# Optimization experiments

Measured on AMD Instinct MI355X. Metric: run time of the kernel, lower is better.

Reference implementation:

```python
import jax, jax.numpy as jnp
import numpy as np

DIM = 128
NUM_HEADS = 4
HEAD_DIM = DIM // NUM_HEADS
SCALE = HEAD_DIM ** -0.5


def setup_inputs() -> dict:
    key = jax.random.key(0)
    k1, k2, k3, k4, k5, k6 = jax.random.split(key, 6)
    BW, T = 8192, 49  # batch_windows, tokens per 7x7 window
    nW = 64           # distinct window masks; BW % nW == 0
    return {
        "x": jax.random.normal(k1, (BW, T, DIM), dtype=jnp.float32),
        "attention_mask": jax.random.normal(k2, (nW, T, T), dtype=jnp.float32),
        "w_qkv": jax.random.normal(k3, (3 * DIM, DIM), dtype=jnp.float32) * 0.02,
        "b_qkv": jax.random.normal(k4, (3 * DIM,), dtype=jnp.float32) * 0.02,
        "w_proj": jax.random.normal(k5, (DIM, DIM), dtype=jnp.float32) * 0.02,
        "b_proj": jax.random.normal(k6, (DIM,), dtype=jnp.float32) * 0.02,
    }


def reference(x, attention_mask, w_qkv, b_qkv, w_proj, b_proj):
    BW, T, C = x.shape
    H, hd = NUM_HEADS, HEAD_DIM
    # qkv projection: [BW, T, 3C] -> [3, BW, H, T, hd]
    qkv = (x @ w_qkv.T + b_qkv).reshape(BW, T, 3, H, hd)
    qkv = jnp.transpose(qkv, (2, 0, 3, 1, 4))
    q, k, v = qkv[0], qkv[1], qkv[2]
    # scaled dot-product scores: [BW, H, T, T]
    attn = jnp.einsum("bhqd,bhkd->bhqk", q * SCALE, k)
    nW = attention_mask.shape[0]
    # broadcast-add per-window mask over (batch, heads)
    attn = attn.reshape(-1, nW, H, T, T) + attention_mask[None, :, None, :, :]
    attn = attn.reshape(BW, H, T, T)
    attn = jax.nn.softmax(attn, axis=-1)
    out = jnp.einsum("bhqk,bhkd->bhqd", attn, v)  # [BW, H, T, hd]
    out = jnp.swapaxes(out, 1, 2).reshape(BW, T, C)
    return out @ w_proj.T + b_proj
```

## Files before the change

### kernel.cpp

```cpp
#include <hip/hip_runtime.h>
#include <hip/hip_bf16.h>


#define T49  49
#define CDIM 128
#define NW   64
#define SCALEF 0.17677669529663689f

typedef short bf16x8 __attribute__((ext_vector_type(8)));
typedef float f32x4  __attribute__((ext_vector_type(4)));

union B8 { unsigned int u[4]; bf16x8 v; };

__device__ __forceinline__ unsigned int pk2(float a, float b) {
  __hip_bfloat162 h = __float22bfloat162_rn(make_float2(a, b));
  unsigned int u;
  __builtin_memcpy(&u, &h, 4);
  return u;
}

__device__ __forceinline__ unsigned short f2bf(float f) {
  unsigned int u = __builtin_bit_cast(unsigned int, f);
  u += 0x7fffu + ((u >> 16) & 1u);
  return (unsigned short)(u >> 16);
}

__global__ void prep_kernel(const float* __restrict__ wq, const float* __restrict__ wp,
                            const float* __restrict__ mask,
                            short* __restrict__ wq_bf, short* __restrict__ wp_bf,
                            float* __restrict__ maskp) {
  const int i = blockIdx.x * 256 + threadIdx.x;
  const int w = i >> 12, q = (i >> 6) & 63, k = i & 63;
  float val = -3.0e38f;
  if (q < T49 && k < T49) val = mask[(w * T49 + q) * T49 + k];
  float rm = val;
  rm = fmaxf(rm, __shfl_xor(rm, 1, 64));
  rm = fmaxf(rm, __shfl_xor(rm, 2, 64));
  rm = fmaxf(rm, __shfl_xor(rm, 4, 64));
  rm = fmaxf(rm, __shfl_xor(rm, 8, 64));
  rm = fmaxf(rm, __shfl_xor(rm, 16, 64));
  rm = fmaxf(rm, __shfl_xor(rm, 32, 64));
  float mv;
  if (q >= T49)      mv = 0.0f;
  else if (k >= T49) mv = -1e30f;
  else               mv = val - rm;
  maskp[i] = mv;
  if (i < 3 * CDIM * CDIM) wq_bf[i] = (short)f2bf(wq[i]);
  if (i < CDIM * CDIM)     wp_bf[i] = (short)f2bf(wp[i]);
}

__global__ __launch_bounds__(256)
__attribute__((amdgpu_waves_per_eu(4, 4)))
void winattn_kernel(const float* __restrict__ x, const float* __restrict__ maskp,
                    const float* __restrict__ b_qkv, const float* __restrict__ b_proj,
                    const short* __restrict__ wq, const short* __restrict__ wp,
                    float* __restrict__ out) {
  __shared__ __align__(16) char smem[32768];
  constexpr int Q_BASE = 0, KO_BASE = 16384;

  const int bw    = blockIdx.x;
  const int wv    = threadIdx.x >> 6;
  const int lane  = threadIdx.x & 63;
  const int g     = lane >> 4;
  const int j16   = lane & 15;
  const int wmask = bw & (NW - 1);

  bf16x8 xa[4][4];
#pragma unroll
  for (int tt = 0; tt < 4; ++tt) {
    const int t = tt * 16 + j16;
#pragma unroll
    for (int kt = 0; kt < 4; ++kt) {
      B8 u;
      if (t < T49) {
        const float* p = x + (size_t)bw * (T49 * CDIM) + t * CDIM + kt * 32 + g * 8;
        const float4 v0 = *(const float4*)p;
        const float4 v1 = *(const float4*)(p + 4);
        u.u[0] = pk2(v0.x, v0.y); u.u[1] = pk2(v0.z, v0.w);
        u.u[2] = pk2(v1.x, v1.y); u.u[3] = pk2(v1.z, v1.w);
      } else {
        u.u[0] = u.u[1] = u.u[2] = u.u[3] = 0u;
      }
      xa[tt][kt] = u.v;
    }
  }

  unsigned int pkV[2][4][2];

#pragma unroll
  for (int ni = 0; ni < 6; ++ni) {
    const int ct = (ni < 2) ? (wv * 2 + ni)
                 : (ni < 4) ? (8 + wv * 2 + (ni - 2))
                            : (16 + wv * 2 + (ni - 4));
    bf16x8 wf[4];
#pragma unroll
    for (int kt = 0; kt < 4; ++kt)
      wf[kt] = *(const bf16x8*)(wq + (ct * 16 + j16) * CDIM + kt * 32 + g * 8);

    if (ni < 4) {
      const int  c0  = ct * 16 + g * 4;
      const bool isQ = (ni < 2);
      float4 b4 = *(const float4*)(b_qkv + c0);
      const float sc = isQ ? SCALEF : 1.0f;
      const int d0 = c0 & 31;
      char* base = smem + (isQ ? Q_BASE : KO_BASE) + wv * 4096;
#pragma unroll
      for (int tt = 0; tt < 4; ++tt) {
        f32x4 acc = {0.f, 0.f, 0.f, 0.f};
#pragma unroll
        for (int kt = 0; kt < 4; ++kt)
          acc = __builtin_amdgcn_mfma_f32_16x16x32_bf16(wf[kt], xa[tt][kt], acc, 0, 0, 0);
        const int t = tt * 16 + j16;
        const uint2 w2 = make_uint2(pk2(fmaf(acc[0], sc, b4.x * sc), fmaf(acc[1], sc, b4.y * sc)),
                                    pk2(fmaf(acc[2], sc, b4.z * sc), fmaf(acc[3], sc, b4.w * sc)));
        *(uint2*)(base + t * 64 + ((d0 * 2) ^ ((t & 3) << 4))) = w2;
      }
    } else {
      const int   vi   = ni - 4;
      const float bias = b_qkv[ct * 16 + j16];
#pragma unroll
      for (int tt = 0; tt < 4; ++tt) {
        f32x4 acc = {0.f, 0.f, 0.f, 0.f};
#pragma unroll
        for (int kt = 0; kt < 4; ++kt)
          acc = __builtin_amdgcn_mfma_f32_16x16x32_bf16(xa[tt][kt], wf[kt], acc, 0, 0, 0);
        pkV[vi][tt][0] = pk2(acc[0] + bias, acc[1] + bias);
        pkV[vi][tt][1] = pk2(acc[2] + bias, acc[3] + bias);
      }
    }
  }

  const int gh   = g >> 1;
  const int srcA = (((2 * g    ) & 3) << 4) | j16;
  const int srcB = (((2 * g + 1) & 3) << 4) | j16;

  const char* Kb = smem + KO_BASE + wv * 4096;
  const char* Qb = smem + Q_BASE  + wv * 4096;
  bf16x8 kb[4], qb[4];
#pragma unroll
  for (int mt = 0; mt < 4; ++mt) {
    const int t = mt * 16 + j16;
    kb[mt] = *(const bf16x8*)(Kb + t * 64 + ((g * 16) ^ ((t & 3) << 4)));
    qb[mt] = *(const bf16x8*)(Qb + t * 64 + ((g * 16) ^ ((t & 3) << 4)));
  }

  bf16x8 va[2][2];
#pragma unroll
  for (int dt = 0; dt < 2; ++dt)
#pragma unroll
    for (int ks = 0; ks < 2; ++ks) {
      const unsigned int a0  = (unsigned)__shfl((int)pkV[dt][2 * ks    ][0], srcA, 64);
      const unsigned int a0h = (unsigned)__shfl((int)pkV[dt][2 * ks + 1][0], srcA, 64);
      const unsigned int a1  = (unsigned)__shfl((int)pkV[dt][2 * ks    ][1], srcA, 64);
      const unsigned int a1h = (unsigned)__shfl((int)pkV[dt][2 * ks + 1][1], srcA, 64);
      const unsigned int b0  = (unsigned)__shfl((int)pkV[dt][2 * ks    ][0], srcB, 64);
      const unsigned int b0h = (unsigned)__shfl((int)pkV[dt][2 * ks + 1][0], srcB, 64);
      const unsigned int b1  = (unsigned)__shfl((int)pkV[dt][2 * ks    ][1], srcB, 64);
      const unsigned int b1h = (unsigned)__shfl((int)pkV[dt][2 * ks + 1][1], srcB, 64);
      B8 u;
      u.u[0] = gh ? a0h : a0;
      u.u[1] = gh ? a1h : a1;
      u.u[2] = gh ? b0h : b0;
      u.u[3] = gh ? b1h : b1;
      va[dt][ks] = u.v;
    }

  __syncthreads();

  char*        Ob  = smem + KO_BASE;
  const float* mwb = maskp + wmask * 4096;

#pragma unroll
  for (int nt = 0; nt < 4; ++nt) {
    const float* mp = mwb + (nt * 16 + j16) * 64 + g * 4;
    float4 m4[4];
#pragma unroll
    for (int mt = 0; mt < 4; ++mt) m4[mt] = *(const float4*)(mp + mt * 16);

    const f32x4 zero = {0.f, 0.f, 0.f, 0.f};
    float v[4][4];
#pragma unroll
    for (int mt = 0; mt < 4; ++mt) {
      const f32x4 s = __builtin_amdgcn_mfma_f32_16x16x32_bf16(kb[mt], qb[nt], zero, 0, 0, 0);
      v[mt][0] = __expf(s[0] + m4[mt].x); v[mt][1] = __expf(s[1] + m4[mt].y);
      v[mt][2] = __expf(s[2] + m4[mt].z); v[mt][3] = __expf(s[3] + m4[mt].w);
    }
    float sr[8];
#pragma unroll
    for (int mt = 0; mt < 4; ++mt) {
      sr[2 * mt]     = v[mt][0] + v[mt][1];
      sr[2 * mt + 1] = v[mt][2] + v[mt][3];
    }
    float sum = ((sr[0] + sr[1]) + (sr[2] + sr[3])) + ((sr[4] + sr[5]) + (sr[6] + sr[7]));
    sum += __shfl_xor(sum, 16, 64);
    sum += __shfl_xor(sum, 32, 64);
    const float inv = 1.0f / sum;

    unsigned int pkn[4][2];
#pragma unroll
    for (int mt = 0; mt < 4; ++mt) {
      pkn[mt][0] = pk2(v[mt][0], v[mt][1]);
      pkn[mt][1] = pk2(v[mt][2], v[mt][3]);
    }

    f32x4 oacc[2] = {{0.f,0.f,0.f,0.f},{0.f,0.f,0.f,0.f}};
#pragma unroll
    for (int ks = 0; ks < 2; ++ks) {
      const unsigned int p00 = (unsigned)__shfl((int)pkn[2*ks  ][0], srcA, 64);
      const unsigned int p10 = (unsigned)__shfl((int)pkn[2*ks+1][0], srcA, 64);
      const unsigned int p01 = (unsigned)__shfl((int)pkn[2*ks  ][1], srcA, 64);
      const unsigned int p11 = (unsigned)__shfl((int)pkn[2*ks+1][1], srcA, 64);
      const unsigned int q00 = (unsigned)__shfl((int)pkn[2*ks  ][0], srcB, 64);
      const unsigned int q10 = (unsigned)__shfl((int)pkn[2*ks+1][0], srcB, 64);
      const unsigned int q01 = (unsigned)__shfl((int)pkn[2*ks  ][1], srcB, 64);
      const unsigned int q11 = (unsigned)__shfl((int)pkn[2*ks+1][1], srcB, 64);
      B8 bf;
      bf.u[0] = gh ? p10 : p00;
      bf.u[1] = gh ? p11 : p01;
      bf.u[2] = gh ? q10 : q00;
      bf.u[3] = gh ? q11 : q01;
#pragma unroll
      for (int dt = 0; dt < 2; ++dt)
        oacc[dt] = __builtin_amdgcn_mfma_f32_16x16x32_bf16(va[dt][ks], bf.v, oacc[dt], 0, 0, 0);
    }

    const int to = nt * 16 + j16;
    const int sw = (to & 7) << 5;
#pragma unroll
    for (int dt = 0; dt < 2; ++dt) {
      const int ch0 = wv * 32 + dt * 16 + g * 4;
      const uint2 w2 = make_uint2(pk2(oacc[dt][0] * inv, oacc[dt][1] * inv),
                                  pk2(oacc[dt][2] * inv, oacc[dt][3] * inv));
      *(uint2*)(Ob + to * 256 + ((ch0 * 2) ^ sw)) = w2;
    }
  }
  __syncthreads();

  {
    const char* Ob2 = smem + KO_BASE;
    bf16x8 oa[4][4];
#pragma unroll
    for (int mt = 0; mt < 4; ++mt) {
      const int t = mt * 16 + j16;
      const int sw = (t & 7) << 5;
#pragma unroll
      for (int kt = 0; kt < 4; ++kt)
        oa[mt][kt] = *(const bf16x8*)(Ob2 + t * 256 + ((kt * 64 + g * 16) ^ sw));
    }
    float* ob = out + (size_t)bw * (T49 * CDIM);
#pragma unroll
    for (int ntl = 0; ntl < 2; ++ntl) {
      const int c = (wv * 2 + ntl) * 16 + j16;
      bf16x8 bfr[4];
#pragma unroll
      for (int kt = 0; kt < 4; ++kt)
        bfr[kt] = *(const bf16x8*)(wp + c * CDIM + kt * 32 + g * 8);
      const float bias = b_proj[c];
#pragma unroll
      for (int mt = 0; mt < 4; ++mt) {
        f32x4 acc = {0.f, 0.f, 0.f, 0.f};
#pragma unroll
        for (int kt = 0; kt < 4; ++kt)
          acc = __builtin_amdgcn_mfma_f32_16x16x32_bf16(oa[mt][kt], bfr[kt], acc, 0, 0, 0);
#pragma unroll
        for (int r = 0; r < 4; ++r) {
          const int t = mt * 16 + g * 4 + r;
          if (t < T49) ob[t * CDIM + c] = acc[r] + bias;
        }
      }
    }
  }
}

extern "C" void kernel_launch(void* const* d_in, const int* in_sizes, int n_in,
                              void* d_out, int out_size, void* d_ws, size_t ws_size,
                              hipStream_t stream) {
  const float* x      = (const float*)d_in[0];
  const float* mask   = (const float*)d_in[1];
  const float* w_qkv  = (const float*)d_in[2];
  const float* b_qkv  = (const float*)d_in[3];
  const float* w_proj = (const float*)d_in[4];
  const float* b_proj = (const float*)d_in[5];
  float* out = (float*)d_out;

  float* maskp = (float*)d_ws;
  short* wq_bf = (short*)((char*)d_ws + 64*64*64*4);
  short* wp_bf = wq_bf + 3 * CDIM * CDIM;

  hipLaunchKernelGGL(prep_kernel, dim3(1024), dim3(256), 0, stream,
                     w_qkv, w_proj, mask, wq_bf, wp_bf, maskp);
  hipLaunchKernelGGL(winattn_kernel, dim3(8192), dim3(256), 0, stream,
                     x, maskp, b_qkv, b_proj, wq_bf, wp_bf, out);
}
```

Baseline: 294.3 us.

## Stage x in LDS, move Q/K via shuffles, fold bias and mask into MFMA

The x tile is now converted to bf16 once and staged in a swizzled 16 KB LDS buffer instead of being held in registers. Q and K fragments are exchanged with cross-lane shuffles rather than through shared memory. The attention scale is folded into the bf16 Q weights during prep, and the biases and mask are passed as MFMA accumulator inputs. Together with the smaller LDS footprint and a relaxed waves-per-EU hint, this aims to cut register and LDS pressure and raise occupancy, at the cost of more shuffles and a block-wide barrier before the QKV projection.

```diff
diff --git a/kernel.cpp b/kernel.cpp
--- a/kernel.cpp
+++ b/kernel.cpp
@@ -45,18 +45,21 @@
   else if (k >= T49) mv = -1e30f;
   else               mv = val - rm;
   maskp[i] = mv;
-  if (i < 3 * CDIM * CDIM) wq_bf[i] = (short)f2bf(wq[i]);
-  if (i < CDIM * CDIM)     wp_bf[i] = (short)f2bf(wp[i]);
+  if (i < 3 * CDIM * CDIM) {
+    float wv_ = wq[i];
+    if (i < CDIM * CDIM) wv_ *= SCALEF;
+    wq_bf[i] = (short)f2bf(wv_);
+  }
+  if (i < CDIM * CDIM) wp_bf[i] = (short)f2bf(wp[i]);
 }
 
 __global__ __launch_bounds__(256)
-__attribute__((amdgpu_waves_per_eu(4, 4)))
+__attribute__((amdgpu_waves_per_eu(5)))
 void winattn_kernel(const float* __restrict__ x, const float* __restrict__ maskp,
                     const float* __restrict__ b_qkv, const float* __restrict__ b_proj,
                     const short* __restrict__ wq, const short* __restrict__ wp,
                     float* __restrict__ out) {
-  __shared__ __align__(16) char smem[32768];
-  constexpr int Q_BASE = 0, KO_BASE = 16384;
+  __shared__ __align__(16) char smem[16384];
 
   const int bw    = blockIdx.x;
   const int wv    = threadIdx.x >> 6;
@@ -65,26 +68,38 @@
   const int j16   = lane & 15;
   const int wmask = bw & (NW - 1);
 
-  bf16x8 xa[4][4];
-#pragma unroll
-  for (int tt = 0; tt < 4; ++tt) {
+  {
+    const int tid = threadIdx.x;
+    const int t   = tid >> 2;
+    const int c0  = (tid & 3) * 32;
+    char* wb = smem + t * 256;
+    const int swz = (t & 7) << 4;
+    if (t < T49) {
+      const float* p = x + (size_t)bw * (T49 * CDIM) + t * CDIM + c0;
+#pragma unroll
+      for (int q = 0; q < 4; ++q) {
+        const float4 v0 = *(const float4*)(p + q * 8);
+        const float4 v1 = *(const float4*)(p + q * 8 + 4);
+        uint4 u;
+        u.x = pk2(v0.x, v0.y); u.y = pk2(v0.z, v0.w);
+        u.z = pk2(v1.x, v1.y); u.w = pk2(v1.z, v1.w);
+        *(uint4*)(wb + ((c0 * 2 + q * 16) ^ swz)) = u;
+      }
+    } else {
+#pragma unroll
+      for (int q = 0; q < 4; ++q)
+        *(uint4*)(wb + ((c0 * 2 + q * 16) ^ swz)) = make_uint4(0u, 0u, 0u, 0u);
+    }
+  }
+  __syncthreads();
+
+  auto XF = [&](int tt, int kt) -> bf16x8 {
     const int t = tt * 16 + j16;
-#pragma unroll
-    for (int kt = 0; kt < 4; ++kt) {
-      B8 u;
-      if (t < T49) {
-        const float* p = x + (size_t)bw * (T49 * CDIM) + t * CDIM + kt * 32 + g * 8;
-        const float4 v0 = *(const float4*)p;
-        const float4 v1 = *(const float4*)(p + 4);
-        u.u[0] = pk2(v0.x, v0.y); u.u[1] = pk2(v0.z, v0.w);
-        u.u[2] = pk2(v1.x, v1.y); u.u[3] = pk2(v1.z, v1.w);
-      } else {
-        u.u[0] = u.u[1] = u.u[2] = u.u[3] = 0u;
-      }
-      xa[tt][kt] = u.v;
-    }
-  }
-
+    return *(const bf16x8*)(smem + t * 256 + ((kt * 64 + g * 16) ^ ((t & 7) << 4)));
+  };
+
+  unsigned int pkQ[2][4][2];
+  unsigned int pkK[2][4][2];
   unsigned int pkV[2][4][2];
 
 #pragma unroll
@@ -98,34 +113,35 @@
       wf[kt] = *(const bf16x8*)(wq + (ct * 16 + j16) * CDIM + kt * 32 + g * 8);
 
     if (ni < 4) {
-      const int  c0  = ct * 16 + g * 4;
-      const bool isQ = (ni < 2);
+      const int   c0 = ct * 16 + g * 4;
       float4 b4 = *(const float4*)(b_qkv + c0);
-      const float sc = isQ ? SCALEF : 1.0f;
-      const int d0 = c0 & 31;
-      char* base = smem + (isQ ? Q_BASE : KO_BASE) + wv * 4096;
+      if (ni < 2) { b4.x *= SCALEF; b4.y *= SCALEF; b4.z *= SCALEF; b4.w *= SCALEF; }
+      const f32x4 cin = {b4.x, b4.y, b4.z, b4.w};
 #pragma unroll
       for (int tt = 0; tt < 4; ++tt) {
-        f32x4 acc = {0.f, 0.f, 0.f, 0.f};
+        f32x4 acc = cin;
 #pragma unroll
         for (int kt = 0; kt < 4; ++kt)
-          acc = __builtin_amdgcn_mfma_f32_16x16x32_bf16(wf[kt], xa[tt][kt], acc, 0, 0, 0);
-        const int t = tt * 16 + j16;
-        const uint2 w2 = make_uint2(pk2(fmaf(acc[0], sc, b4.x * sc), fmaf(acc[1], sc, b4.y * sc)),
-                                    pk2(fmaf(acc[2], sc, b4.z * sc), fmaf(acc[3], sc, b4.w * sc)));
-        *(uint2*)(base + t * 64 + ((d0 * 2) ^ ((t & 3) << 4))) = w2;
+          acc = __builtin_amdgcn_mfma_f32_16x16x32_bf16(wf[kt], XF(tt, kt), acc, 0, 0, 0);
+        unsigned int p0 = pk2(acc[0], acc[1]);
+        unsigned int p1 = pk2(acc[2], acc[3]);
+        if (ni == 0)      { pkQ[0][tt][0] = p0; pkQ[0][tt][1] = p1; }
+        else if (ni == 1) { pkQ[1][tt][0] = p0; pkQ[1][tt][1] = p1; }
+        else if (ni == 2) { pkK[0][tt][0] = p0; pkK[0][tt][1] = p1; }
+        else              { pkK[1][tt][0] = p0; pkK[1][tt][1] = p1; }
       }
     } else {
       const int   vi   = ni - 4;
       const float bias = b_qkv[ct * 16 + j16];
+      const f32x4 cin = {bias, bias, bias, bias};
 #pragma unroll
       for (int tt = 0; tt < 4; ++tt) {
-        f32x4 acc = {0.f, 0.f, 0.f, 0.f};
+        f32x4 acc = cin;
 #pragma unroll
         for (int kt = 0; kt < 4; ++kt)
-          acc = __builtin_amdgcn_mfma_f32_16x16x32_bf16(xa[tt][kt], wf[kt], acc, 0, 0, 0);
-        pkV[vi][tt][0] = pk2(acc[0] + bias, acc[1] + bias);
-        pkV[vi][tt][1] = pk2(acc[2] + bias, acc[3] + bias);
+          acc = __builtin_amdgcn_mfma_f32_16x16x32_bf16(XF(tt, kt), wf[kt], acc, 0, 0, 0);
+        pkV[vi][tt][0] = pk2(acc[0], acc[1]);
+        pkV[vi][tt][1] = pk2(acc[2], acc[3]);
       }
     }
   }
@@ -134,14 +150,41 @@
   const int srcA = (((2 * g    ) & 3) << 4) | j16;
   const int srcB = (((2 * g + 1) & 3) << 4) | j16;
 
-  const char* Kb = smem + KO_BASE + wv * 4096;
-  const char* Qb = smem + Q_BASE  + wv * 4096;
-  bf16x8 kb[4], qb[4];
+  bf16x8 qb[4], kb[4];
 #pragma unroll
   for (int mt = 0; mt < 4; ++mt) {
-    const int t = mt * 16 + j16;
-    kb[mt] = *(const bf16x8*)(Kb + t * 64 + ((g * 16) ^ ((t & 3) << 4)));
-    qb[mt] = *(const bf16x8*)(Qb + t * 64 + ((g * 16) ^ ((t & 3) << 4)));
+    {
+      const unsigned int a0 = (unsigned)__shfl((int)pkQ[0][mt][0], srcA, 64);
+      const unsigned int a1 = (unsigned)__shfl((int)pkQ[0][mt][1], srcA, 64);
+      const unsigned int c0 = (unsigned)__shfl((int)pkQ[1][mt][0], srcA, 64);
+      const unsigned int c1 = (unsigned)__shfl((int)pkQ[1][mt][1], srcA, 64);
+      const unsigned int b0 = (unsigned)__shfl((int)pkQ[0][mt][0], srcB, 64);
+      const unsigned int b1 = (unsigned)__shfl((int)pkQ[0][mt][1], srcB, 64);
+      const unsigned int d0 = (unsigned)__shfl((int)pkQ[1][mt][0], srcB, 64);
+      const unsigned int d1 = (unsigned)__shfl((int)pkQ[1][mt][1], srcB, 64);
+      B8 u;
+      u.u[0] = gh ? c0 : a0;
+      u.u[1] = gh ? c1 : a1;
+      u.u[2] = gh ? d0 : b0;
+      u.u[3] = gh ? d1 : b1;
+      qb[mt] = u.v;
+    }
+    {
+      const unsigned int a0 = (unsigned)__shfl((int)pkK[0][mt][0], srcA, 64);
+      const unsigned int a1 = (unsigned)__shfl((int)pkK[0][mt][1], srcA, 64);
+      const unsigned int c0 = (unsigned)__shfl((int)pkK[1][mt][0], srcA, 64);
+      const unsigned int c1 = (unsigned)__shfl((int)pkK[1][mt][1], srcA, 64);
+      const unsigned int b0 = (unsigned)__shfl((int)pkK[0][mt][0], srcB, 64);
+      const unsigned int b1 = (unsigned)__shfl((int)pkK[0][mt][1], srcB, 64);
+      const unsigned int d0 = (unsigned)__shfl((int)pkK[1][mt][0], srcB, 64);
+      const unsigned int d1 = (unsigned)__shfl((int)pkK[1][mt][1], srcB, 64);
+      B8 u;
+      u.u[0] = gh ? c0 : a0;
+      u.u[1] = gh ? c1 : a1;
+      u.u[2] = gh ? d0 : b0;
+      u.u[3] = gh ? d1 : b1;
+      kb[mt] = u.v;
+    }
   }
 
   bf16x8 va[2][2];
@@ -167,23 +210,20 @@
 
   __syncthreads();
 
-  char*        Ob  = smem + KO_BASE;
+  char*        Ob  = smem;
   const float* mwb = maskp + wmask * 4096;
 
 #pragma unroll
   for (int nt = 0; nt < 4; ++nt) {
     const float* mp = mwb + (nt * 16 + j16) * 64 + g * 4;
-    float4 m4[4];
-#pragma unroll
-    for (int mt = 0; mt < 4; ++mt) m4[mt] = *(const float4*)(mp + mt * 16);
-
-    const f32x4 zero = {0.f, 0.f, 0.f, 0.f};
     float v[4][4];
 #pragma unroll
     for (int mt = 0; mt < 4; ++mt) {
-      const f32x4 s = __builtin_amdgcn_mfma_f32_16x16x32_bf16(kb[mt], qb[nt], zero, 0, 0, 0);
-      v[mt][0] = __expf(s[0] + m4[mt].x); v[mt][1] = __expf(s[1] + m4[mt].y);
-      v[mt][2] = __expf(s[2] + m4[mt].z); v[mt][3] = __expf(s[3] + m4[mt].w);
+      const float4 m4 = *(const float4*)(mp + mt * 16);
+      const f32x4 cin = {m4.x, m4.y, m4.z, m4.w};
+      const f32x4 s = __builtin_amdgcn_mfma_f32_16x16x32_bf16(kb[mt], qb[nt], cin, 0, 0, 0);
+      v[mt][0] = __expf(s[0]); v[mt][1] = __expf(s[1]);
+      v[mt][2] = __expf(s[2]); v[mt][3] = __expf(s[3]);
     }
     float sr[8];
 #pragma unroll
@@ -237,7 +277,7 @@
   __syncthreads();
 
   {
-    const char* Ob2 = smem + KO_BASE;
+    const char* Ob2 = smem;
     bf16x8 oa[4][4];
 #pragma unroll
     for (int mt = 0; mt < 4; ++mt) {
```

Result: slower. 858.7 us (+191.7%).
